# Performance work log

Measured on AMD Instinct MI355X. Metric: run time of the kernel, lower is better.

## Reference

```python
import jax, jax.numpy as jnp
import numpy as np

B, S, E, H, L, D, G, V = 32, 256, 300, 256, 4000, 256, 512, 50000
LIN1, LIN2 = 512, 256  # linear_size


def _glorot(key, shape):
    fan_in, fan_out = shape[-1], shape[-2] if len(shape) > 1 else shape[-1]
    std = np.sqrt(2.0 / (fan_in + fan_out))
    return jax.random.normal(key, shape, dtype=jnp.float32) * std


def setup_inputs() -> dict:
    key = jax.random.key(0)
    ks = jax.random.split(key, 20)
    tokens = jax.random.randint(ks[0], (B, S), 1, V)  # avoid padding_idx=0
    emb_table = jax.random.normal(ks[1], (V, E), dtype=jnp.float32) * 0.1
    emb_table = emb_table.at[0].set(0.0)  # padding row
    # bidirectional LSTM (1 layer), torch gate order i,f,g,o
    w_ih_f = _glorot(ks[2], (4 * H, E));  w_hh_f = _glorot(ks[3], (4 * H, H))
    b_f = jnp.zeros((4 * H,), jnp.float32)
    w_ih_b = _glorot(ks[4], (4 * H, E));  w_hh_b = _glorot(ks[5], (4 * H, H))
    b_b = jnp.zeros((4 * H,), jnp.float32)
    # MLAttention: Linear(2H -> L, bias=False)
    attn_w = _glorot(ks[6], (L, 2 * H))
    # label graph branch
    label_emb = _glorot(ks[7], (L, D))
    adj_raw = (jax.random.uniform(ks[8], (L, L)) < 0.004).astype(jnp.float32)
    adj_raw = adj_raw + jnp.eye(L, dtype=jnp.float32)
    deg = jnp.sum(adj_raw, axis=1, keepdims=True)
    adj = adj_raw / deg  # row-normalized dense adjacency [L, L]
    gcn_w = _glorot(ks[9], (D, G));  gcn_b = jnp.zeros((G,), jnp.float32)
    # MLLinear([2H+G, 512, 256], 1)
    w1 = _glorot(ks[10], (2 * H + G, LIN1));  b1 = jnp.zeros((LIN1,), jnp.float32)
    w2 = _glorot(ks[11], (LIN1, LIN2));       b2 = jnp.zeros((LIN2,), jnp.float32)
    w_out = _glorot(ks[12], (LIN2, 1));       b_out = jnp.zeros((1,), jnp.float32)
    return dict(tokens=tokens, emb_table=emb_table,
                w_ih_f=w_ih_f, w_hh_f=w_hh_f, b_f=b_f,
                w_ih_b=w_ih_b, w_hh_b=w_hh_b, b_b=b_b,
                attn_w=attn_w, label_emb=label_emb, adj=adj,
                gcn_w=gcn_w, gcn_b=gcn_b,
                w1=w1, b1=b1, w2=w2, b2=b2, w_out=w_out, b_out=b_out)


def _lstm_dir(x_gates, w_hh, reverse):
    # x_gates: [B, S, 4H] precomputed input projections (+bias)
    def step(carry, xt):
        h, c = carry
        gates = xt + h @ w_hh.T
        i, f, g, o = jnp.split(gates, 4, axis=-1)
        c = jax.nn.sigmoid(f) * c + jax.nn.sigmoid(i) * jnp.tanh(g)
        h = jax.nn.sigmoid(o) * jnp.tanh(c)
        return (h, c), h
    b = x_gates.shape[0]
    init = (jnp.zeros((b, H), x_gates.dtype), jnp.zeros((b, H), x_gates.dtype))
    _, hs = jax.lax.scan(step, init, jnp.swapaxes(x_gates, 0, 1), reverse=reverse)
    return jnp.swapaxes(hs, 0, 1)  # [B, S, H]


def reference(tokens, emb_table, w_ih_f, w_hh_f, b_f, w_ih_b, w_hh_b, b_b,
              attn_w, label_emb, adj, gcn_w, gcn_b,
              w1, b1, w2, b2, w_out, b_out):
    masks = tokens != 0  # [B, S]
    emb_out = emb_table[tokens]  # [B, S, E]
    # bidirectional LSTM -> [B, S, 2H]
    gates_f = jnp.einsum('bse,ge->bsg', emb_out, w_ih_f) + b_f
    gates_b = jnp.einsum('bse,ge->bsg', emb_out, w_ih_b) + b_b
    rnn_out = jnp.concatenate([_lstm_dir(gates_f, w_hh_f, False),
                               _lstm_dir(gates_b, w_hh_b, True)], axis=-1)
    # MLAttention: per-label attention over sequence
    scores = jnp.einsum('bsh,lh->bls', rnn_out, attn_w)  # [B, L, S]
    scores = jnp.where(masks[:, None, :], scores, jnp.float32(-1e9))
    attn = jax.nn.softmax(scores, axis=-1)
    attn_out = jnp.einsum('bls,bsh->blh', attn, rnn_out)  # [B, L, 2H]
    # GCN over label graph: relu(A @ (X W) + b), single layer [D -> G]
    gcn_out = jax.nn.relu(adj @ (label_emb @ gcn_w) + gcn_b)  # [L, G]
    gcn_out = jnp.broadcast_to(gcn_out[None], (attn_out.shape[0], L, G))
    # concat fusion + MLLinear([2H+G, 512, 256], 1)
    x = jnp.concatenate([attn_out, gcn_out], axis=-1)  # [B, L, 2H+G]
    x = jax.nn.relu(x @ w1 + b1)
    x = jax.nn.relu(x @ w2 + b2)
    out = jnp.squeeze(x @ w_out + b_out, -1)  # [B, L]
    return out
```

## Files before the change

### kernel.cpp

```cpp
#include <hip/hip_runtime.h>
#include <hip/hip_bf16.h>
#include <math.h>


typedef __attribute__((ext_vector_type(8))) short bfrag;
typedef __attribute__((ext_vector_type(4))) float ffrag;

__device__ __forceinline__ ushort f2bf(float x) {
    union { float f; unsigned u; } c; c.f = x;
    const unsigned r = c.u + 0x7fffu + ((c.u >> 16) & 1u);
    return (ushort)(r >> 16);
}
__device__ __forceinline__ float bf2f(ushort h) {
    union { unsigned u; float f; } c; c.u = (unsigned)h << 16;
    return c.f;
}

template<bool BT, bool GATHER>
__global__ __launch_bounds__(256) void gemm_k(
    const float* __restrict__ A, const float* __restrict__ Bm, float* __restrict__ C,
    int M, int N, int K, int lda, int ldb, int ldc,
    long abs_, long bbs_, long cbs_,
    const int* __restrict__ tok,
    const float* __restrict__ bias,
    const float* __restrict__ addrow, int addmod, int ldadd,
    int do_relu)
{
    const int tid = threadIdx.x;
    const int tx = tid & 15;
    const int ty = tid >> 4;
    const int n0 = blockIdx.x * 128;
    const int m0 = blockIdx.y * 64;
    const int z  = blockIdx.z;
    A  += (size_t)z * abs_;
    Bm += (size_t)z * bbs_;
    C  += (size_t)z * cbs_;

    __shared__ float As[16][68];
    __shared__ float Bs[16][132];

    float acc[4][8];
#pragma unroll
    for (int i = 0; i < 4; ++i)
#pragma unroll
        for (int j = 0; j < 8; ++j) acc[i][j] = 0.f;

    const int ksteps = (K + 15) / 16;
    for (int kt = 0; kt < ksteps; ++kt) {
        const int k0 = kt * 16;
#pragma unroll
        for (int j = 0; j < 4; ++j) {
            int e  = tid + j * 256;
            int kk = e & 15;
            int m  = e >> 4;
            int gm = m0 + m, gk = k0 + kk;
            float v = 0.f;
            if (gm < M && gk < K) {
                size_t rb;
                if (GATHER) rb = (size_t)tok[gm] * lda;
                else        rb = (size_t)gm * lda;
                v = A[rb + gk];
            }
            As[kk][m] = v;
        }
#pragma unroll
        for (int j = 0; j < 8; ++j) {
            int e = tid + j * 256;
            if (BT) {
                int kk = e & 15;
                int n  = e >> 4;
                int gn = n0 + n, gk = k0 + kk;
                Bs[kk][n] = (gn < N && gk < K) ? Bm[(size_t)gn * ldb + gk] : 0.f;
            } else {
                int n  = e & 127;
                int kk = e >> 7;
                int gn = n0 + n, gk = k0 + kk;
                Bs[kk][n] = (gn < N && gk < K) ? Bm[(size_t)gk * ldb + gn] : 0.f;
            }
        }
        __syncthreads();
#pragma unroll
        for (int kk = 0; kk < 16; ++kk) {
            const float4 av  = *(const float4*)&As[kk][ty * 4];
            const float4 b0v = *(const float4*)&Bs[kk][tx * 8];
            const float4 b1v = *(const float4*)&Bs[kk][tx * 8 + 4];
            const float a_[4] = {av.x, av.y, av.z, av.w};
            const float b_[8] = {b0v.x, b0v.y, b0v.z, b0v.w, b1v.x, b1v.y, b1v.z, b1v.w};
#pragma unroll
            for (int i = 0; i < 4; ++i)
#pragma unroll
                for (int j = 0; j < 8; ++j) acc[i][j] = fmaf(a_[i], b_[j], acc[i][j]);
        }
        __syncthreads();
    }

#pragma unroll
    for (int i = 0; i < 4; ++i) {
        const int gm = m0 + ty * 4 + i;
        if (gm >= M) continue;
        const float* addp = addrow ? (addrow + (size_t)(gm % addmod) * ldadd) : nullptr;
#pragma unroll
        for (int j = 0; j < 8; ++j) {
            const int gn = n0 + tx * 8 + j;
            if (gn >= N) continue;
            float v = acc[i][j];
            if (bias) v += bias[gn];
            if (addp) v += addp[gn];
            if (do_relu) v = fmaxf(v, 0.f);
            C[(size_t)gm * ldc + gn] = v;
        }
    }
}

template<bool BIAS, bool ADDROW, bool RELU, bool OUTF, bool OUTS>
__global__ __launch_bounds__(256) void mgemm_k(
    const ushort* __restrict__ A, const ushort* __restrict__ B,
    float* __restrict__ Cf, ushort* __restrict__ Cs,
    int M, int N, int K, int lda, int ldb, int ldc, int ldcs,
    long abs_, long bbs_, long cbs_, long csbs_,
    const float* __restrict__ bias,
    const float* __restrict__ addrow, int addmod, int ldadd)
{
    const int tid = threadIdx.x;
    const int ln = tid & 63;
    const int wv = tid >> 6;
    const int wm = wv >> 1, wn = wv & 1;
    const int m0 = blockIdx.x * 128, n0 = blockIdx.y * 128;
    const int z = blockIdx.z;
    A += (size_t)z * abs_;
    B += (size_t)z * bbs_;

    __shared__ ushort Ah[128 * 40], Al[128 * 40], Bh[128 * 40], Bl[128 * 40];

    ffrag acc[4][4];
#pragma unroll
    for (int i = 0; i < 4; ++i)
#pragma unroll
        for (int j = 0; j < 4; ++j) acc[i][j] = ffrag{0.f, 0.f, 0.f, 0.f};

    const int sr = tid >> 1;
    const int sk = (tid & 1) * 16;
    const int am = min(m0 + sr, M - 1);
    const int bn = n0 + sr;
    const int fr = ln & 15;
    const int fk = (ln >> 4) * 8;

    const ushort* arow = A + (size_t)am * lda + sk;
    const ushort* brow = B + (size_t)bn * ldb + sk;

    bfrag ah0, ah1, al0, al1, bh0, bh1, bl0, bl1;
    {
        const ushort* ap = arow;
        const ushort* bp = brow;
        ah0 = *(const bfrag*)ap;       ah1 = *(const bfrag*)(ap + 8);
        al0 = *(const bfrag*)(ap + K); al1 = *(const bfrag*)(ap + K + 8);
        bh0 = *(const bfrag*)bp;       bh1 = *(const bfrag*)(bp + 8);
        bl0 = *(const bfrag*)(bp + K); bl1 = *(const bfrag*)(bp + K + 8);
    }

    for (int k0 = 0; k0 < K; k0 += 32) {
        __syncthreads();
        *(bfrag*)&Ah[sr * 40 + sk] = ah0;  *(bfrag*)&Ah[sr * 40 + sk + 8] = ah1;
        *(bfrag*)&Al[sr * 40 + sk] = al0;  *(bfrag*)&Al[sr * 40 + sk + 8] = al1;
        *(bfrag*)&Bh[sr * 40 + sk] = bh0;  *(bfrag*)&Bh[sr * 40 + sk + 8] = bh1;
        *(bfrag*)&Bl[sr * 40 + sk] = bl0;  *(bfrag*)&Bl[sr * 40 + sk + 8] = bl1;
        __syncthreads();
        if (k0 + 32 < K) {
            const ushort* ap = arow + k0 + 32;
            const ushort* bp = brow + k0 + 32;
            ah0 = *(const bfrag*)ap;       ah1 = *(const bfrag*)(ap + 8);
            al0 = *(const bfrag*)(ap + K); al1 = *(const bfrag*)(ap + K + 8);
            bh0 = *(const bfrag*)bp;       bh1 = *(const bfrag*)(bp + 8);
            bl0 = *(const bfrag*)(bp + K); bl1 = *(const bfrag*)(bp + K + 8);
        }
        bfrag afh[4], afl[4];
#pragma unroll
        for (int i = 0; i < 4; ++i) {
            const int ar = (wm * 64 + i * 16 + fr) * 40 + fk;
            afh[i] = *(const bfrag*)&Ah[ar];
            afl[i] = *(const bfrag*)&Al[ar];
        }
#pragma unroll
        for (int j = 0; j < 4; ++j) {
            const int br = (wn * 64 + j * 16 + fr) * 40 + fk;
            const bfrag bfh = *(const bfrag*)&Bh[br];
            const bfrag bfl = *(const bfrag*)&Bl[br];
#pragma unroll
            for (int i = 0; i < 4; ++i) {
                acc[i][j] = __builtin_amdgcn_mfma_f32_16x16x32_bf16(afh[i], bfh, acc[i][j], 0, 0, 0);
                acc[i][j] = __builtin_amdgcn_mfma_f32_16x16x32_bf16(afh[i], bfl, acc[i][j], 0, 0, 0);
                acc[i][j] = __builtin_amdgcn_mfma_f32_16x16x32_bf16(afl[i], bfh, acc[i][j], 0, 0, 0);
            }
        }
    }

#pragma unroll
    for (int i = 0; i < 4; ++i) {
#pragma unroll
        for (int rg = 0; rg < 4; ++rg) {
            const int gm = m0 + wm * 64 + i * 16 + (ln >> 4) * 4 + rg;
            if (gm >= M) continue;
            const float* addp = ADDROW ? (addrow + (size_t)(gm % addmod) * ldadd) : nullptr;
#pragma unroll
            for (int j = 0; j < 4; ++j) {
                const int gn = n0 + wn * 64 + j * 16 + fr;
                float v = acc[i][j][rg];
                if (BIAS) v += bias[gn];
                if (ADDROW) v += addp[gn];
                if (RELU) v = fmaxf(v, 0.f);
                if (OUTF) Cf[(size_t)z * cbs_ + (size_t)gm * ldc + gn] = v;
                if (OUTS) {
                    const ushort h = f2bf(v);
                    const ushort l = f2bf(v - bf2f(h));
                    ushort* cp = Cs + (size_t)z * csbs_ + (size_t)gm * ldcs;
                    cp[gn] = h;
                    cp[N + gn] = l;
                }
            }
        }
    }
}

__global__ void gsplit_k(const float* __restrict__ src, const int* __restrict__ tok,
                         ushort* __restrict__ outp, int K, int Kpad)
{
    const int r = blockIdx.x;
    const float* s = src + (size_t)(tok ? tok[r] : r) * K;
    ushort* o = outp + (size_t)r * 2 * Kpad;
    for (int k = threadIdx.x; k < Kpad; k += blockDim.x) {
        const float x = (k < K) ? s[k] : 0.f;
        const ushort h = f2bf(x);
        const ushort l = f2bf(x - bf2f(h));
        o[k] = h;
        o[Kpad + k] = l;
    }
}

__global__ void split_k(const float* __restrict__ in, ushort* __restrict__ outp,
                        int rows, int K)
{
    const int i = blockIdx.x * 256 + threadIdx.x;
    if (i >= rows * K) return;
    const int r = i / K, k = i - r * K;
    const float x = in[i];
    const ushort h = f2bf(x);
    const ushort l = f2bf(x - bf2f(h));
    ushort* o = outp + (size_t)r * 2 * K;
    o[k] = h;
    o[K + k] = l;
}

__global__ __launch_bounds__(256) void tsplit_k(
    const float* __restrict__ in, ushort* __restrict__ outp,
    int R, int C, int ldin, long ibs, long obs)
{
    __shared__ float t[64][65];
    const int c0 = blockIdx.x * 64, r0 = blockIdx.y * 64;
    in   += (size_t)blockIdx.z * ibs;
    outp += (size_t)blockIdx.z * obs;
    const int tx = threadIdx.x & 15, ty = threadIdx.x >> 4;
#pragma unroll
    for (int i = 0; i < 4; ++i) {
        const int r = ty * 4 + i;
        const float4 v = *(const float4*)&in[(size_t)(r0 + r) * ldin + c0 + tx * 4];
        t[tx * 4 + 0][r] = v.x;
        t[tx * 4 + 1][r] = v.y;
        t[tx * 4 + 2][r] = v.z;
        t[tx * 4 + 3][r] = v.w;
    }
    __syncthreads();
    const int R2 = 2 * R;
#pragma unroll
    for (int i = 0; i < 4; ++i) {
        const int c = ty * 4 + i;
        ushort h[4], l[4];
#pragma unroll
        for (int k2 = 0; k2 < 4; ++k2) {
            const float x = t[c][tx * 4 + k2];
            h[k2] = f2bf(x);
            l[k2] = f2bf(x - bf2f(h[k2]));
        }
        uint2 hw, lw;
        hw.x = (unsigned)h[0] | ((unsigned)h[1] << 16);
        hw.y = (unsigned)h[2] | ((unsigned)h[3] << 16);
        lw.x = (unsigned)l[0] | ((unsigned)l[1] << 16);
        lw.y = (unsigned)l[2] | ((unsigned)l[3] << 16);
        *(uint2*)&outp[(size_t)(c0 + c) * R2 + r0 + tx * 4] = hw;
        *(uint2*)&outp[(size_t)(c0 + c) * R2 + R + r0 + tx * 4] = lw;
    }
}

__global__ __launch_bounds__(1024) void lstm_reg_k(
    const float* __restrict__ gxf, const float* __restrict__ gxb,
    const float* __restrict__ whf, const float* __restrict__ whb,
    float* __restrict__ rnn, float* hbuf, int* stamp)
{
    const int p = blockIdx.x;
    const int q = blockIdx.y;
    const int b = p >> 1, dir = p & 1;
    const float* xg = dir ? gxb : gxf;
    const float* W  = dir ? whb : whf;
    const int tid = threadIdx.x;
    const int wv = tid >> 6, lane = tid & 63;
    const int ul = lane >> 4;
    const int ks = (lane >> 2) & 3;
    const int gt = lane & 3;
    const int u  = wv * 4 + ul;
    const int grow = gt * 256 + q * 64 + u;

    float4 w[16];
    {
        const float4* wp = (const float4*)(W + (size_t)grow * 256 + ks * 64);
#pragma unroll
        for (int i = 0; i < 16; ++i) w[i] = wp[i];
    }

    __shared__ float h_lds[4 * 68];
    __shared__ float xg_lds[320];

    float* hb0 = hbuf + (size_t)p * 256;
    float* hb1 = hbuf + (size_t)(64 + p) * 256;
    int* sp = stamp + p * 16;

    const size_t xgb = (size_t)b * 256;
    const int g2 = (tid >> 6) * 256 + q * 64 + (tid & 63);
    float c = 0.f;
    float xg_cur = 0.f;
    if (tid < 256) xg_cur = xg[(xgb + (dir ? 255 : 0)) * 1024 + g2];

    for (int st = 0; st < 256; ++st) {
        const int ts = dir ? 255 - st : st;
        if (st > 0 && tid == 0) {
            while (true) {
                int s0 = __hip_atomic_load(&sp[0], __ATOMIC_RELAXED, __HIP_MEMORY_SCOPE_AGENT);
                int s1 = __hip_atomic_load(&sp[1], __ATOMIC_RELAXED, __HIP_MEMORY_SCOPE_AGENT);
                int s2 = __hip_atomic_load(&sp[2], __ATOMIC_RELAXED, __HIP_MEMORY_SCOPE_AGENT);
                int s3 = __hip_atomic_load(&sp[3], __ATOMIC_RELAXED, __HIP_MEMORY_SCOPE_AGENT);
                if (min(min(s0, s1), min(s2, s3)) >= st) break;
            }
        }
        __syncthreads();
        if (tid < 256) {
            float hv = 0.f;
            if (st > 0) {
                const float* src = (st & 1) ? hb0 : hb1;
                hv = __hip_atomic_load(&src[tid], __ATOMIC_RELAXED, __HIP_MEMORY_SCOPE_AGENT);
            }
            h_lds[(tid >> 6) * 68 + (tid & 63)] = hv;
            xg_lds[(tid & 63) * 5 + (tid >> 6)] = xg_cur;
        }
        __syncthreads();
        float acc = 0.f;
        {
            const float4* hp = (const float4*)&h_lds[ks * 68];
#pragma unroll
            for (int i = 0; i < 16; ++i) {
                const float4 hv = hp[i];
                acc = fmaf(w[i].x, hv.x, acc);
                acc = fmaf(w[i].y, hv.y, acc);
                acc = fmaf(w[i].z, hv.z, acc);
                acc = fmaf(w[i].w, hv.w, acc);
            }
        }
        acc += __shfl_xor(acc, 4);
        acc += __shfl_xor(acc, 8);
        const float g = acc + xg_lds[u * 5 + gt];
        const float t1 = __shfl_xor(g, 1);
        const float t2 = __shfl_xor(g, 2);
        const float t3 = __shfl_xor(t1, 2);
        const float g0 = (gt == 0) ? g : (gt == 1) ? t1 : (gt == 2) ? t2 : t3;
        const float g1 = (gt == 1) ? g : (gt == 0) ? t1 : (gt == 3) ? t2 : t3;
        const float g2v = (gt == 2) ? g : (gt == 3) ? t1 : (gt == 0) ? t2 : t3;
        const float g3v = (gt == 3) ? g : (gt == 2) ? t1 : (gt == 1) ? t2 : t3;
        const float si = 1.f / (1.f + __expf(-g0));
        const float sf = 1.f / (1.f + __expf(-g1));
        const float so = 1.f / (1.f + __expf(-g3v));
        const float tg = 1.f - 2.f / (__expf(2.f * g2v) + 1.f);
        c = sf * c + si * tg;
        const float tc = 1.f - 2.f / (__expf(2.f * c) + 1.f);
        const float hn = so * tc;
        if ((lane & 15) == 0) {
            float* dst = (st & 1) ? hb1 : hb0;
            __hip_atomic_store(&dst[q * 64 + u], hn, __ATOMIC_RELAXED, __HIP_MEMORY_SCOPE_AGENT);
            rnn[(xgb + ts) * 512 + (size_t)dir * 256 + q * 64 + u] = hn;
        }
        __syncthreads();
        if (tid == 0) {
            __hip_atomic_store(&sp[q], st + 1, __ATOMIC_RELAXED, __HIP_MEMORY_SCOPE_AGENT);
        }
        if (tid < 256 && st < 255) {
            const int tsn = dir ? 254 - st : st + 1;
            xg_cur = xg[(xgb + tsn) * 1024 + g2];
        }
    }
}

__global__ void init_cnt_k(int* stamp) {
    const int i = blockIdx.x * blockDim.x + threadIdx.x;
    if (i < 1024) stamp[i] = 0;
}

__global__ __launch_bounds__(256) void softmax_split_k(
    float* __restrict__ sc, const int* __restrict__ tokens, int b0)
{
    const int bb = blockIdx.y;
    const int l  = blockIdx.x * 4 + (threadIdx.x >> 6);
    const int lane = threadIdx.x & 63;
    float* row = sc + ((size_t)bb * 4000 + l) * 256;
    const int* tk = tokens + (size_t)(b0 + bb) * 256;
    float4 v = *(const float4*)&row[lane * 4];
    const int4 tv = *(const int4*)&tk[lane * 4];
    if (tv.x == 0) v.x = -1e9f;
    if (tv.y == 0) v.y = -1e9f;
    if (tv.z == 0) v.z = -1e9f;
    if (tv.w == 0) v.w = -1e9f;
    float mx = fmaxf(fmaxf(v.x, v.y), fmaxf(v.z, v.w));
    for (int o = 32; o > 0; o >>= 1) mx = fmaxf(mx, __shfl_xor(mx, o));
    v.x = __expf(v.x - mx); v.y = __expf(v.y - mx);
    v.z = __expf(v.z - mx); v.w = __expf(v.w - mx);
    float s = v.x + v.y + v.z + v.w;
    for (int o = 32; o > 0; o >>= 1) s += __shfl_xor(s, o);
    const float inv = 1.f / s;
    const float p0 = v.x * inv, p1 = v.y * inv, p2 = v.z * inv, p3 = v.w * inv;
    const ushort h0 = f2bf(p0), h1 = f2bf(p1), h2 = f2bf(p2), h3 = f2bf(p3);
    const ushort l0 = f2bf(p0 - bf2f(h0)), l1 = f2bf(p1 - bf2f(h1));
    const ushort l2 = f2bf(p2 - bf2f(h2)), l3 = f2bf(p3 - bf2f(h3));
    ushort* orow = (ushort*)row;
    uint2 hw, lw;
    hw.x = (unsigned)h0 | ((unsigned)h1 << 16);
    hw.y = (unsigned)h2 | ((unsigned)h3 << 16);
    lw.x = (unsigned)l0 | ((unsigned)l1 << 16);
    lw.y = (unsigned)l2 | ((unsigned)l3 << 16);
    *(uint2*)&orow[lane * 4] = hw;
    *(uint2*)&orow[256 + lane * 4] = lw;
}

__global__ __launch_bounds__(256) void spmm_k(
    const float* __restrict__ adj, const float* __restrict__ tmp,
    const float* __restrict__ bias, float* __restrict__ outp)
{
    const int l = blockIdx.x;
    __shared__ int   idxs[4][256];
    __shared__ float vals[4][256];
    __shared__ int   cnts[4];
    const int t = threadIdx.x;
    const int w = t >> 6, lane = t & 63;
    const float* arow = adj + (size_t)l * 4000;
    int cnt = 0;
    for (int r = 0; r < 16; ++r) {
        const int o = r * 64 + lane;
        const int j = w * 1000 + o;
        const float a = (o < 1000) ? arow[j] : 0.f;
        const unsigned long long mk = __ballot(a != 0.f);
        if (a != 0.f) {
            const int pos = cnt + __popcll(mk & ((1ull << lane) - 1ull));
            if (pos < 256) { idxs[w][pos] = j; vals[w][pos] = a; }
        }
        cnt += __popcll(mk);
    }
    if (lane == 0) cnts[w] = min(cnt, 256);
    __syncthreads();
    const int c0 = t * 2;
    float a0 = 0.f, a1 = 0.f;
    for (int ww = 0; ww < 4; ++ww) {
        const int n = cnts[ww];
        for (int e = 0; e < n; ++e) {
            const float a = vals[ww][e];
            const float2 tv = *(const float2*)&tmp[(size_t)idxs[ww][e] * 512 + c0];
            a0 = fmaf(a, tv.x, a0);
            a1 = fmaf(a, tv.y, a1);
        }
    }
    float2 res;
    res.x = fmaxf(a0 + bias[c0], 0.f);
    res.y = fmaxf(a1 + bias[c0 + 1], 0.f);
    *(float2*)&outp[(size_t)l * 512 + c0] = res;
}

__global__ __launch_bounds__(256) void out_k(
    const float* __restrict__ x2, const float* __restrict__ w_out,
    const float* __restrict__ b_out, float* __restrict__ outp, int b0)
{
    const int r = blockIdx.x * 4 + (threadIdx.x >> 6);
    const int lane = threadIdx.x & 63;
    const float4 xv = *(const float4*)&x2[(size_t)r * 256 + lane * 4];
    const float4 wv = *(const float4*)&w_out[lane * 4];
    float s = xv.x * wv.x + xv.y * wv.y + xv.z * wv.z + xv.w * wv.w;
    for (int o = 32; o > 0; o >>= 1) s += __shfl_xor(s, o);
    if (lane == 0) {
        const int bb = r / 4000, l = r - bb * 4000;
        outp[(size_t)(b0 + bb) * 4000 + l] = s + b_out[0];
    }
}

extern "C" void kernel_launch(void* const* d_in, const int* in_sizes, int n_in,
                              void* d_out, int out_size, void* d_ws, size_t ws_size,
                              hipStream_t stream)
{
    const int*   tokens    = (const int*)  d_in[0];
    const float* emb       = (const float*)d_in[1];
    const float* w_ih_f    = (const float*)d_in[2];
    const float* w_hh_f    = (const float*)d_in[3];
    const float* b_f       = (const float*)d_in[4];
    const float* w_ih_b    = (const float*)d_in[5];
    const float* w_hh_b    = (const float*)d_in[6];
    const float* b_b       = (const float*)d_in[7];
    const float* attn_w    = (const float*)d_in[8];
    const float* label_emb = (const float*)d_in[9];
    const float* adj       = (const float*)d_in[10];
    const float* gcn_w     = (const float*)d_in[11];
    const float* gcn_b     = (const float*)d_in[12];
    const float* w1        = (const float*)d_in[13];
    const float* b1        = (const float*)d_in[14];
    const float* w2        = (const float*)d_in[15];
    const float* b2        = (const float*)d_in[16];
    const float* w_out     = (const float*)d_in[17];
    const float* b_out     = (const float*)d_in[18];
    float* outp = (float*)d_out;
    float* wsf  = (float*)d_ws;

    const size_t off_gf  = 0;
    const size_t off_gb  = 8388608;
    const size_t off_rnn = 16777216;
    const size_t off_tmp = 20971520;
    const size_t off_go  = 23019520;
    const size_t off_ctr = 25067520;
    const size_t base_end = 27115520;
    const size_t S_sz = 10829824;
    const size_t have = ws_size / 4;
    int NB = 1; size_t offS = off_gf, offC = off_gf + S_sz;
    {
        const int tiers[6] = {32, 16, 8, 4, 2, 0};
        bool found = false;
        for (int t = 0; tiers[t]; ++t) {
            if (have >= base_end + S_sz + (size_t)tiers[t] * 5120000) {
                NB = tiers[t]; offS = base_end; offC = base_end + S_sz; found = true; break;
            }
        }
        if (!found && have >= base_end + S_sz) { NB = 2; offS = base_end; offC = off_gf; }
    }

    float* gates_f = wsf + off_gf;
    float* gates_b = wsf + off_gb;
    float* rnn     = wsf + off_rnn;
    float* gcn_tmp = wsf + off_tmp;
    float* gcn_out = wsf + off_go;
    float* contrib = wsf + off_ctr;
    float* hbuf    = wsf + off_tmp;
    int*   stamp   = (int*)(wsf + off_tmp + 32768);

    const size_t off_esp = (offS == off_gf) ? off_rnn : offS;
    ushort* esplit  = (ushort*)(wsf + off_esp);
    ushort* wsplitf = esplit + (size_t)8192 * 640;
    ushort* wsplitb = wsplitf + (size_t)1024 * 640;

    ushort* attn_ws16 = (ushort*)(wsf + offS);
    ushort* w1t16     = (ushort*)(wsf + offS + 2048000);
    ushort* w2t16     = (ushort*)(wsf + offS + 2310144);
    ushort* rnn_nt16  = (ushort*)(wsf + offS + 2441216);
    ushort* rnnT16    = (ushort*)(wsf + offS + 6635520);

    float*  scoresb = wsf + offC;
    ushort* attn16  = (ushort*)(wsf + offC + (size_t)NB * 1024000);
    ushort* x116    = (ushort*)(wsf + offC + (size_t)NB * 1024000 + (size_t)NB * 2048000);
    float*  x2b     = scoresb;

    init_cnt_k<<<4, 256, 0, stream>>>(stamp);

    gsplit_k<<<8192, 256, 0, stream>>>(emb, tokens, esplit, 300, 320);
    gsplit_k<<<1024, 256, 0, stream>>>(w_ih_f, nullptr, wsplitf, 300, 320);
    gsplit_k<<<1024, 256, 0, stream>>>(w_ih_b, nullptr, wsplitb, 300, 320);
    mgemm_k<true, false, false, true, false><<<dim3(64, 8, 1), 256, 0, stream>>>(
        esplit, wsplitf, gates_f, nullptr,
        8192, 1024, 320, 640, 640, 1024, 0,
        0L, 0L, 0L, 0L, b_f, nullptr, 1, 0);
    mgemm_k<true, false, false, true, false><<<dim3(64, 8, 1), 256, 0, stream>>>(
        esplit, wsplitb, gates_b, nullptr,
        8192, 1024, 320, 640, 640, 1024, 0,
        0L, 0L, 0L, 0L, b_b, nullptr, 1, 0);

    lstm_reg_k<<<dim3(64, 4), 1024, 0, stream>>>(
        gates_f, gates_b, w_hh_f, w_hh_b, rnn, hbuf, stamp);

    split_k<<<16384, 256, 0, stream>>>(rnn, rnn_nt16, 8192, 512);
    tsplit_k<<<dim3(8, 4, 32), 256, 0, stream>>>(rnn, rnnT16, 256, 512, 512, 131072, 262144);
    split_k<<<8000, 256, 0, stream>>>(attn_w, attn_ws16, 4000, 512);
    tsplit_k<<<dim3(8, 8, 1), 256, 0, stream>>>(w1, w1t16, 512, 512, 512, 0, 0);
    tsplit_k<<<dim3(4, 8, 1), 256, 0, stream>>>(w2, w2t16, 512, 256, 256, 0, 0);

    gemm_k<false, false><<<dim3(4, 63, 1), 256, 0, stream>>>(
        label_emb, gcn_w, gcn_tmp, 4000, 512, 256, 256, 512, 512,
        0, 0, 0, nullptr, nullptr, nullptr, 1, 0, 0);
    spmm_k<<<dim3(4000), 256, 0, stream>>>(adj, gcn_tmp, gcn_b, gcn_out);
    gemm_k<false, false><<<dim3(4, 63, 1), 256, 0, stream>>>(
        gcn_out, w1 + (size_t)512 * 512, contrib, 4000, 512, 512, 512, 512, 512,
        0, 0, 0, nullptr, b1, nullptr, 1, 0, 0);

    for (int b0 = 0; b0 < 32; b0 += NB) {
        const int nb = (32 - b0 < NB) ? (32 - b0) : NB;
        mgemm_k<false, false, false, true, false><<<dim3(32, 2, nb), 256, 0, stream>>>(
            attn_ws16, rnn_nt16 + (size_t)b0 * 262144, scoresb, nullptr,
            4000, 256, 512, 1024, 1024, 256, 0,
            0L, 262144L, 1024000L, 0L, nullptr, nullptr, 1, 0);
        softmax_split_k<<<dim3(1000, nb), 256, 0, stream>>>(scoresb, tokens, b0);
        mgemm_k<false, false, false, false, true><<<dim3(32, 4, nb), 256, 0, stream>>>(
            (const ushort*)scoresb, rnnT16 + (size_t)b0 * 262144, nullptr, attn16,
            4000, 512, 256, 512, 512, 0, 1024,
            2048000L, 262144L, 0L, 4096000L, nullptr, nullptr, 1, 0);
        mgemm_k<false, true, true, false, true><<<dim3((nb * 4000 + 127) / 128, 4, 1), 256, 0, stream>>>(
            attn16, w1t16, nullptr, x116,
            nb * 4000, 512, 512, 1024, 1024, 0, 1024,
            0L, 0L, 0L, 0L, nullptr, contrib, 4000, 512);
        mgemm_k<true, false, true, true, false><<<dim3((nb * 4000 + 127) / 128, 2, 1), 256, 0, stream>>>(
            x116, w2t16, x2b, nullptr,
            nb * 4000, 256, 512, 1024, 1024, 256, 0,
            0L, 0L, 0L, 0L, b2, nullptr, 1, 0);
        out_k<<<dim3(nb * 1000), 256, 0, stream>>>(x2b, w_out, b_out, outp, b0);
    }
}
```

Before: 1.967 ms.

## Tag LSTM hidden-state words with step stamps and move GCN GEMMs to MFMA

The LSTM cross-block handoff drops the separate per-block stamp array and its spin/barrier pair. Each hidden value is now written as a 64-bit word carrying the step number, and readers spin per element until the tag matches. This removes one __syncthreads and a serialized poll by thread 0 on every step of the 256-step recurrence, at the cost of doubled hbuf traffic and per-thread spinning. Separately, the two fp32 SIMT GEMMs in the GCN branch are replaced with split-bf16 MFMA GEMMs, which adds extra split/transpose kernels.

```diff
diff --git a/kernel.cpp b/kernel.cpp
--- a/kernel.cpp
+++ b/kernel.cpp
@@ -14,102 +14,6 @@
 __device__ __forceinline__ float bf2f(ushort h) {
     union { unsigned u; float f; } c; c.u = (unsigned)h << 16;
     return c.f;
-}
-
-template<bool BT, bool GATHER>
-__global__ __launch_bounds__(256) void gemm_k(
-    const float* __restrict__ A, const float* __restrict__ Bm, float* __restrict__ C,
-    int M, int N, int K, int lda, int ldb, int ldc,
-    long abs_, long bbs_, long cbs_,
-    const int* __restrict__ tok,
-    const float* __restrict__ bias,
-    const float* __restrict__ addrow, int addmod, int ldadd,
-    int do_relu)
-{
-    const int tid = threadIdx.x;
-    const int tx = tid & 15;
-    const int ty = tid >> 4;
-    const int n0 = blockIdx.x * 128;
-    const int m0 = blockIdx.y * 64;
-    const int z  = blockIdx.z;
-    A  += (size_t)z * abs_;
-    Bm += (size_t)z * bbs_;
-    C  += (size_t)z * cbs_;
-
-    __shared__ float As[16][68];
-    __shared__ float Bs[16][132];
-
-    float acc[4][8];
-#pragma unroll
-    for (int i = 0; i < 4; ++i)
-#pragma unroll
-        for (int j = 0; j < 8; ++j) acc[i][j] = 0.f;
-
-    const int ksteps = (K + 15) / 16;
-    for (int kt = 0; kt < ksteps; ++kt) {
-        const int k0 = kt * 16;
-#pragma unroll
-        for (int j = 0; j < 4; ++j) {
-            int e  = tid + j * 256;
-            int kk = e & 15;
-            int m  = e >> 4;
-            int gm = m0 + m, gk = k0 + kk;
-            float v = 0.f;
-            if (gm < M && gk < K) {
-                size_t rb;
-                if (GATHER) rb = (size_t)tok[gm] * lda;
-                else        rb = (size_t)gm * lda;
-                v = A[rb + gk];
-            }
-            As[kk][m] = v;
-        }
-#pragma unroll
-        for (int j = 0; j < 8; ++j) {
-            int e = tid + j * 256;
-            if (BT) {
-                int kk = e & 15;
-                int n  = e >> 4;
-                int gn = n0 + n, gk = k0 + kk;
-                Bs[kk][n] = (gn < N && gk < K) ? Bm[(size_t)gn * ldb + gk] : 0.f;
-            } else {
-                int n  = e & 127;
-                int kk = e >> 7;
-                int gn = n0 + n, gk = k0 + kk;
-                Bs[kk][n] = (gn < N && gk < K) ? Bm[(size_t)gk * ldb + gn] : 0.f;
-            }
-        }
-        __syncthreads();
-#pragma unroll
-        for (int kk = 0; kk < 16; ++kk) {
-            const float4 av  = *(const float4*)&As[kk][ty * 4];
-            const float4 b0v = *(const float4*)&Bs[kk][tx * 8];
-            const float4 b1v = *(const float4*)&Bs[kk][tx * 8 + 4];
-            const float a_[4] = {av.x, av.y, av.z, av.w};
-            const float b_[8] = {b0v.x, b0v.y, b0v.z, b0v.w, b1v.x, b1v.y, b1v.z, b1v.w};
-#pragma unroll
-            for (int i = 0; i < 4; ++i)
-#pragma unroll
-                for (int j = 0; j < 8; ++j) acc[i][j] = fmaf(a_[i], b_[j], acc[i][j]);
-        }
-        __syncthreads();
-    }
-
-#pragma unroll
-    for (int i = 0; i < 4; ++i) {
-        const int gm = m0 + ty * 4 + i;
-        if (gm >= M) continue;
-        const float* addp = addrow ? (addrow + (size_t)(gm % addmod) * ldadd) : nullptr;
-#pragma unroll
-        for (int j = 0; j < 8; ++j) {
-            const int gn = n0 + tx * 8 + j;
-            if (gn >= N) continue;
-            float v = acc[i][j];
-            if (bias) v += bias[gn];
-            if (addp) v += addp[gn];
-            if (do_relu) v = fmaxf(v, 0.f);
-            C[(size_t)gm * ldc + gn] = v;
-        }
-    }
 }
 
 template<bool BIAS, bool ADDROW, bool RELU, bool OUTF, bool OUTS>
@@ -293,7 +197,7 @@
 __global__ __launch_bounds__(1024) void lstm_reg_k(
     const float* __restrict__ gxf, const float* __restrict__ gxb,
     const float* __restrict__ whf, const float* __restrict__ whb,
-    float* __restrict__ rnn, float* hbuf, int* stamp)
+    float* __restrict__ rnn, unsigned long long* hbuf)
 {
     const int p = blockIdx.x;
     const int q = blockIdx.y;
@@ -318,9 +222,8 @@
     __shared__ float h_lds[4 * 68];
     __shared__ float xg_lds[320];
 
-    float* hb0 = hbuf + (size_t)p * 256;
-    float* hb1 = hbuf + (size_t)(64 + p) * 256;
-    int* sp = stamp + p * 16;
+    unsigned long long* hb0 = hbuf + (size_t)p * 256;
+    unsigned long long* hb1 = hbuf + (size_t)(64 + p) * 256;
 
     const size_t xgb = (size_t)b * 256;
     const int g2 = (tid >> 6) * 256 + q * 64 + (tid & 63);
@@ -330,21 +233,16 @@
 
     for (int st = 0; st < 256; ++st) {
         const int ts = dir ? 255 - st : st;
-        if (st > 0 && tid == 0) {
-            while (true) {
-                int s0 = __hip_atomic_load(&sp[0], __ATOMIC_RELAXED, __HIP_MEMORY_SCOPE_AGENT);
-                int s1 = __hip_atomic_load(&sp[1], __ATOMIC_RELAXED, __HIP_MEMORY_SCOPE_AGENT);
-                int s2 = __hip_atomic_load(&sp[2], __ATOMIC_RELAXED, __HIP_MEMORY_SCOPE_AGENT);
-                int s3 = __hip_atomic_load(&sp[3], __ATOMIC_RELAXED, __HIP_MEMORY_SCOPE_AGENT);
-                if (min(min(s0, s1), min(s2, s3)) >= st) break;
-            }
-        }
-        __syncthreads();
         if (tid < 256) {
             float hv = 0.f;
             if (st > 0) {
-                const float* src = (st & 1) ? hb0 : hb1;
-                hv = __hip_atomic_load(&src[tid], __ATOMIC_RELAXED, __HIP_MEMORY_SCOPE_AGENT);
+                unsigned long long* src = (st & 1) ? hb0 : hb1;
+                unsigned long long wd;
+                do {
+                    wd = __hip_atomic_load(&src[tid], __ATOMIC_RELAXED, __HIP_MEMORY_SCOPE_AGENT);
+                } while ((unsigned)(wd >> 32) != (unsigned)st);
+                union { unsigned uu; float f; } cv; cv.uu = (unsigned)wd;
+                hv = cv.f;
             }
             h_lds[(tid >> 6) * 68 + (tid & 63)] = hv;
             xg_lds[(tid & 63) * 5 + (tid >> 6)] = xg_cur;
@@ -365,6 +263,7 @@
         acc += __shfl_xor(acc, 4);
         acc += __shfl_xor(acc, 8);
         const float g = acc + xg_lds[u * 5 + gt];
+        __syncthreads();
         const float t1 = __shfl_xor(g, 1);
         const float t2 = __shfl_xor(g, 2);
         const float t3 = __shfl_xor(t1, 2);
@@ -380,13 +279,12 @@
         const float tc = 1.f - 2.f / (__expf(2.f * c) + 1.f);
         const float hn = so * tc;
         if ((lane & 15) == 0) {
-            float* dst = (st & 1) ? hb1 : hb0;
-            __hip_atomic_store(&dst[q * 64 + u], hn, __ATOMIC_RELAXED, __HIP_MEMORY_SCOPE_AGENT);
+            unsigned long long* dst = (st & 1) ? hb1 : hb0;
+            union { float f; unsigned uu; } hv2; hv2.f = hn;
+            const unsigned long long wd =
+                ((unsigned long long)(unsigned)(st + 1) << 32) | (unsigned long long)hv2.uu;
+            __hip_atomic_store(&dst[q * 64 + u], wd, __ATOMIC_RELAXED, __HIP_MEMORY_SCOPE_AGENT);
             rnn[(xgb + ts) * 512 + (size_t)dir * 256 + q * 64 + u] = hn;
-        }
-        __syncthreads();
-        if (tid == 0) {
-            __hip_atomic_store(&sp[q], st + 1, __ATOMIC_RELAXED, __HIP_MEMORY_SCOPE_AGENT);
         }
         if (tid < 256 && st < 255) {
             const int tsn = dir ? 254 - st : st + 1;
@@ -395,9 +293,9 @@
     }
 }
 
-__global__ void init_cnt_k(int* stamp) {
-    const int i = blockIdx.x * blockDim.x + threadIdx.x;
-    if (i < 1024) stamp[i] = 0;
+__global__ void init_hbuf_k(unsigned long long* hbuf) {
+    const int i = blockIdx.x * 256 + threadIdx.x;
+    if (i < 32768) hbuf[i] = 0ull;
 }
 
 __global__ __launch_bounds__(256) void softmax_split_k(
@@ -546,8 +444,7 @@
     float* gcn_tmp = wsf + off_tmp;
     float* gcn_out = wsf + off_go;
     float* contrib = wsf + off_ctr;
-    float* hbuf    = wsf + off_tmp;
-    int*   stamp   = (int*)(wsf + off_tmp + 32768);
+    unsigned long long* hbuf = (unsigned long long*)(wsf + off_tmp);
 
     const size_t off_esp = (offS == off_gf) ? off_rnn : offS;
     ushort* esplit  = (ushort*)(wsf + off_esp);
@@ -565,7 +462,12 @@
     ushort* x116    = (ushort*)(wsf + offC + (size_t)NB * 1024000 + (size_t)NB * 2048000);
     float*  x2b     = scoresb;
 
-    init_cnt_k<<<4, 256, 0, stream>>>(stamp);
+    ushort* le16   = (ushort*)(wsf + offC);
+    ushort* gw16   = le16 + (size_t)4000 * 512;
+    ushort* go16   = gw16 + (size_t)512 * 512;
+    ushort* w1b16  = go16 + (size_t)4000 * 1024;
+
+    init_hbuf_k<<<128, 256, 0, stream>>>(hbuf);
 
     gsplit_k<<<8192, 256, 0, stream>>>(emb, tokens, esplit, 300, 320);
     gsplit_k<<<1024, 256, 0, stream>>>(w_ih_f, nullptr, wsplitf, 300, 320);
@@ -580,7 +482,7 @@
         0L, 0L, 0L, 0L, b_b, nullptr, 1, 0);
 
     lstm_reg_k<<<dim3(64, 4), 1024, 0, stream>>>(
-        gates_f, gates_b, w_hh_f, w_hh_b, rnn, hbuf, stamp);
+        gates_f, gates_b, w_hh_f, w_hh_b, rnn, hbuf);
 
     split_k<<<16384, 256, 0, stream>>>(rnn, rnn_nt16, 8192, 512);
     tsplit_k<<<dim3(8, 4, 32), 256, 0, stream>>>(rnn, rnnT16, 256, 512, 512, 131072, 262144);
@@ -588,13 +490,19 @@
     tsplit_k<<<dim3(8, 8, 1), 256, 0, stream>>>(w1, w1t16, 512, 512, 512, 0, 0);
     tsplit_k<<<dim3(4, 8, 1), 256, 0, stream>>>(w2, w2t16, 512, 256, 256, 0, 0);
 
-    gemm_k<false, false><<<dim3(4, 63, 1), 256, 0, stream>>>(
-        label_emb, gcn_w, gcn_tmp, 4000, 512, 256, 256, 512, 512,
-        0, 0, 0, nullptr, nullptr, nullptr, 1, 0, 0);
+    split_k<<<4000, 256, 0, stream>>>(label_emb, le16, 4000, 256);
+    tsplit_k<<<dim3(8, 4, 1), 256, 0, stream>>>(gcn_w, gw16, 256, 512, 512, 0, 0);
+    mgemm_k<false, false, false, true, false><<<dim3(32, 4, 1), 256, 0, stream>>>(
+        le16, gw16, gcn_tmp, nullptr,
+        4000, 512, 256, 512, 512, 512, 0,
+        0L, 0L, 0L, 0L, nullptr, nullptr, 1, 0);
     spmm_k<<<dim3(4000), 256, 0, stream>>>(adj, gcn_tmp, gcn_b, gcn_out);
-    gemm_k<false, false><<<dim3(4, 63, 1), 256, 0, stream>>>(
-        gcn_out, w1 + (size_t)512 * 512, contrib, 4000, 512, 512, 512, 512, 512,
-        0, 0, 0, nullptr, b1, nullptr, 1, 0, 0);
+    split_k<<<8000, 256, 0, stream>>>(gcn_out, go16, 4000, 512);
+    tsplit_k<<<dim3(8, 8, 1), 256, 0, stream>>>(w1 + (size_t)512 * 512, w1b16, 512, 512, 512, 0, 0);
+    mgemm_k<true, false, false, true, false><<<dim3(32, 4, 1), 256, 0, stream>>>(
+        go16, w1b16, contrib, nullptr,
+        4000, 512, 512, 1024, 1024, 512, 0,
+        0L, 0L, 0L, 0L, b1, nullptr, 1, 0);
 
     for (int b0 = 0; b0 < 32; b0 += NB) {
         const int nb = (32 - b0 < NB) ? (32 - b0) : NB;
```

After: 1.745 ms. -11.3%, faster.
